# Kernel optimization log

Measured on AMD Instinct MI355X. Metric: run time of the kernel, lower is better.

Reference implementation:

```python
import jax, jax.numpy as jnp
import numpy as np

B, T, I, H, O = 64, 512, 256, 512, 10


def _init(key, shape, fan):
    k = 1.0 / np.sqrt(fan)
    return jax.random.uniform(key, shape, jnp.float32, -k, k)


def setup_inputs() -> dict:
    key = jax.random.key(0)
    ks = jax.random.split(key, 16)
    return {
        "x": jax.random.normal(ks[0], (B, T, I), jnp.float32),
        # LSTM params (PyTorch gate order: i, f, g, o)
        "lstm_w_ih": _init(ks[1], (4 * H, I), H),
        "lstm_w_hh": _init(ks[2], (4 * H, H), H),
        "lstm_b_ih": _init(ks[3], (4 * H,), H),
        "lstm_b_hh": _init(ks[4], (4 * H,), H),
        # GRU params (gate order: r, z, n)
        "gru_w_ih": _init(ks[5], (3 * H, H), H),
        "gru_w_hh": _init(ks[6], (3 * H, H), H),
        "gru_b_ih": _init(ks[7], (3 * H,), H),
        "gru_b_hh": _init(ks[8], (3 * H,), H),
        # RNN-tanh params
        "rnn_w_ih": _init(ks[9], (H, H), H),
        "rnn_w_hh": _init(ks[10], (H, H), H),
        "rnn_b_ih": _init(ks[11], (H,), H),
        "rnn_b_hh": _init(ks[12], (H,), H),
        # FC head
        "fc_w": _init(ks[13], (O, H), H),
        "fc_b": _init(ks[14], (O,), H),
    }


def _lstm(x, w_ih, w_hh, b_ih, b_hh):
    # Precompute input projections for all timesteps: [T, B, 4H]
    xg = (jnp.einsum('bti,gi->btg', x, w_ih) + b_ih + b_hh).transpose(1, 0, 2)
    h0 = jnp.zeros((x.shape[0], w_hh.shape[1]), x.dtype)

    def step(carry, xt):
        h, c = carry
        g = xt + h @ w_hh.T
        i, f, gg, o = jnp.split(g, 4, axis=-1)
        c = jax.nn.sigmoid(f) * c + jax.nn.sigmoid(i) * jnp.tanh(gg)
        h = jax.nn.sigmoid(o) * jnp.tanh(c)
        return (h, c), h

    _, hs = jax.lax.scan(step, (h0, h0), xg)
    return hs.transpose(1, 0, 2)  # [B, T, H]


def _gru(x, w_ih, w_hh, b_ih, b_hh):
    xg = (jnp.einsum('bti,gi->btg', x, w_ih) + b_ih).transpose(1, 0, 2)  # [T,B,3H]
    h0 = jnp.zeros((x.shape[0], w_hh.shape[1]), x.dtype)

    def step(h, xt):
        hg = h @ w_hh.T + b_hh
        xr, xz, xn = jnp.split(xt, 3, axis=-1)
        hr, hz, hn = jnp.split(hg, 3, axis=-1)
        r = jax.nn.sigmoid(xr + hr)
        z = jax.nn.sigmoid(xz + hz)
        n = jnp.tanh(xn + r * hn)
        h = (1.0 - z) * n + z * h
        return h, h

    _, hs = jax.lax.scan(step, h0, xg)
    return hs.transpose(1, 0, 2)


def _rnn_tanh(x, w_ih, w_hh, b_ih, b_hh):
    xg = (jnp.einsum('bti,gi->btg', x, w_ih) + b_ih + b_hh).transpose(1, 0, 2)
    h0 = jnp.zeros((x.shape[0], w_hh.shape[1]), x.dtype)

    def step(h, xt):
        h = jnp.tanh(xt + h @ w_hh.T)
        return h, h

    _, hs = jax.lax.scan(step, h0, xg)
    return hs.transpose(1, 0, 2)


def reference(x, lstm_w_ih, lstm_w_hh, lstm_b_ih, lstm_b_hh,
              gru_w_ih, gru_w_hh, gru_b_ih, gru_b_hh,
              rnn_w_ih, rnn_w_hh, rnn_b_ih, rnn_b_hh,
              fc_w, fc_b):
    h = _lstm(x, lstm_w_ih, lstm_w_hh, lstm_b_ih, lstm_b_hh)
    h = _gru(h, gru_w_ih, gru_w_hh, gru_b_ih, gru_b_hh)
    h = _rnn_tanh(h, rnn_w_ih, rnn_w_hh, rnn_b_ih, rnn_b_hh)
    last = h[:, -1]  # [B, H]
    return last @ fc_w.T + fc_b  # [B, O]
```

## Files before the change

### kernel.cpp

```cpp
#include <hip/hip_runtime.h>
#include <cstdint>

typedef _Float16 f16;
typedef _Float16 f16x8 __attribute__((ext_vector_type(8)));
typedef float f32x4 __attribute__((ext_vector_type(4)));
typedef unsigned u32;

#define DI static __device__ __forceinline__

constexpr int T = 512, H = 512, Osz = 10;
constexpr int NWG = 256, NTH = 768;
constexpr int GW = 32;
constexpr int GB = 8;
constexpr int BH = 64 * H;
constexpr size_t XH_OFF = 512 * 1024;
constexpr int XH_GRP = 8 * T * 256;

struct __align__(256) GSync { u32 cnt[2]; u32 epoch; u32 pad[61]; };

DI float sigf(float x)   { return 1.f / (1.f + __expf(-x)); }
DI float tanhf_(float x) { return 1.f - 2.f / (__expf(2.f * x) + 1.f); }

DI f16x8 cvt8(const float* p) {
  f16x8 r;
#pragma unroll
  for (int j = 0; j < 8; ++j) r[j] = (f16)p[j];
  return r;
}

DI void pin8(f16x8& v) { asm volatile("" : "+v"(v)); }

DI void st16_sc1(void* p, f16 v) {
  asm volatile("global_store_short %0, %1, off sc1" :: "v"(p), "v"(v));
}
DI void st32_sc1(void* p, u32 v) {
  asm volatile("global_store_dword %0, %1, off sc1" :: "v"(p), "v"(v));
}
DI void st128_sc1(void* p, f16x8 v) {
  asm volatile("global_store_dwordx4 %0, %1, off sc1" :: "v"(p), "v"(v));
}
DI void vm_drain() { asm volatile("s_waitcnt vmcnt(0)" ::: "memory"); }

DI void ld2_sc1(const void* p0, const void* p1, f16x8& a, f16x8& b) {
  asm volatile(
    "global_load_dwordx4 %0, %2, off sc1\n\t"
    "global_load_dwordx4 %1, %3, off sc1\n\t"
    "s_waitcnt vmcnt(0)"
    : "=&v"(a), "=&v"(b)
    : "v"(p0), "v"(p1)
    : "memory");
}

DI void ldrow8(const f16* base, f16x8* A) {
  asm volatile(
    "global_load_dwordx4 %0, %8, off sc1\n\t"
    "global_load_dwordx4 %1, %8, off offset:16 sc1\n\t"
    "global_load_dwordx4 %2, %8, off offset:32 sc1\n\t"
    "global_load_dwordx4 %3, %8, off offset:48 sc1\n\t"
    "global_load_dwordx4 %4, %8, off offset:64 sc1\n\t"
    "global_load_dwordx4 %5, %8, off offset:80 sc1\n\t"
    "global_load_dwordx4 %6, %8, off offset:96 sc1\n\t"
    "global_load_dwordx4 %7, %8, off offset:112 sc1\n\t"
    "s_waitcnt vmcnt(0)"
    : "=&v"(A[0]), "=&v"(A[1]), "=&v"(A[2]), "=&v"(A[3]),
      "=&v"(A[4]), "=&v"(A[5]), "=&v"(A[6]), "=&v"(A[7])
    : "v"(base)
    : "memory");
}

DI void group_barrier(GSync* g, u32 idx, int tid) {
  __syncthreads();
  if (tid == 0) {
    u32 old = __hip_atomic_fetch_add(&g->cnt[idx & 1], 1u,
                                     __ATOMIC_RELAXED, __HIP_MEMORY_SCOPE_AGENT);
    if (old == GW - 1) {
      __hip_atomic_store(&g->cnt[idx & 1], 0u, __ATOMIC_RELAXED, __HIP_MEMORY_SCOPE_AGENT);
      __hip_atomic_store(&g->epoch, idx + 1, __ATOMIC_RELAXED, __HIP_MEMORY_SCOPE_AGENT);
    } else {
      u32 spins = 0;
      while (__hip_atomic_load(&g->epoch, __ATOMIC_RELAXED, __HIP_MEMORY_SCOPE_AGENT) < idx + 1u) {
        __builtin_amdgcn_s_sleep(1);
        if (++spins > 1000000u) break;
      }
    }
  }
  __syncthreads();
}

__global__ __launch_bounds__(NTH, 1) void rnn_all(
    const float* __restrict__ x,
    const float* __restrict__ lwih, const float* __restrict__ lwhh,
    const float* __restrict__ lbih, const float* __restrict__ lbhh,
    const float* __restrict__ gwih, const float* __restrict__ gwhh,
    const float* __restrict__ gbih, const float* __restrict__ gbhh,
    const float* __restrict__ rwih, const float* __restrict__ rwhh,
    const float* __restrict__ rbih, const float* __restrict__ rbhh,
    const float* __restrict__ fcw, const float* __restrict__ fcb,
    float* __restrict__ out, char* __restrict__ ws)
{
  __shared__ __align__(16) u32 HSu[3 * 2048];
  __shared__ float P[12][16][20];
  __shared__ float sb[16][11];

  const int tid  = threadIdx.x;
  const int bid  = blockIdx.x;
  const int grp  = bid & 7;
  const int w32  = bid >> 3;
  const int bg0  = grp * GB;
  const int col0 = w32 * 16;
  const int w    = tid >> 6;
  const int lane = tid & 63;
  const int ln   = lane & 15;
  const int lk   = lane >> 4;

  GSync* gs = reinterpret_cast<GSync*>(ws) + grp;
  f16* HB = reinterpret_cast<f16*>(ws + 4096);
  f16* xh = reinterpret_cast<f16*>(ws + XH_OFF) + (size_t)grp * XH_GRP;

  f16x8 Bw[24];
#pragma unroll
  for (int ks = 16; ks < 24; ++ks) Bw[ks] = (f16x8)(f16)0.f;
  if (w < 4) {
    const int row = w * 512 + col0 + ln;
    const float* ph  = lwhh + (size_t)row * 512 + lk * 8;
    const float* px2 = lwih + (size_t)row * 256 + lk * 8;
#pragma unroll
    for (int ks = 0; ks < 16; ++ks) Bw[ks] = cvt8(ph + ks * 32);
#pragma unroll
    for (int ks = 0; ks < 8;  ++ks) Bw[16 + ks] = cvt8(px2 + ks * 32);
  } else if (w < 7) {
    const int row = (w - 4) * 512 + col0 + ln;
    const float* p = gwih + (size_t)row * 512 + lk * 8;
#pragma unroll
    for (int ks = 0; ks < 16; ++ks) Bw[ks] = cvt8(p + ks * 32);
  } else if (w < 10) {
    const int row = (w - 7) * 512 + col0 + ln;
    const float* p = gwhh + (size_t)row * 512 + lk * 8;
#pragma unroll
    for (int ks = 0; ks < 16; ++ks) Bw[ks] = cvt8(p + ks * 32);
  } else if (w == 10) {
    const float* p = rwhh + (size_t)(col0 + ln) * 512 + lk * 8;
#pragma unroll
    for (int ks = 0; ks < 16; ++ks) Bw[ks] = cvt8(p + ks * 32);
  } else {
    const float* p = rwih + (size_t)(col0 + ln) * 512 + lk * 8;
#pragma unroll
    for (int ks = 0; ks < 16; ++ks) Bw[ks] = cvt8(p + ks * 32);
  }
#pragma unroll
  for (int ks = 0; ks < 24; ++ks) pin8(Bw[ks]);

  for (int i = tid; i < 16 * 11; i += NTH) {
    int c = i / 11, j = i % 11, col = col0 + c;
    float v;
    if (j < 4)       v = lbih[j * 512 + col] + lbhh[j * 512 + col];
    else if (j < 7)  v = gbih[(j - 4) * 512 + col];
    else if (j < 10) v = gbhh[(j - 7) * 512 + col];
    else             v = rbih[col] + rbhh[col];
    sb[c][j] = v;
  }

  {
    const float* xg_ = x + (size_t)bg0 * (T * 256);
    for (int c = w32 * NTH + tid; c < XH_GRP / 8; c += GW * NTH) {
      const float* p = xg_ + (size_t)c * 8;
      f16x8 v;
#pragma unroll
      for (int j = 0; j < 8; ++j) v[j] = (f16)p[j];
      st128_sc1((void*)(xh + (size_t)c * 8), v);
    }
  }
  {
    int i = w32 * NTH + tid;
    if (i < 12288) {
      int buf = i >> 12, r = i & 4095, par = r >> 11, row = (r >> 8) & 7, cu = r & 255;
      void* p = (void*)(HB + (size_t)buf * 2 * BH + (size_t)par * BH
                           + (size_t)(bg0 + row) * H + cu * 2);
      st32_sc1(p, 0u);
    }
  }
  vm_drain();

  group_barrier(gs, 0u, tid);

  float creg = 0.f, hgreg = 0.f;

  const int hbuf = (w < 7) ? 0 : ((w == 10) ? 2 : 1);
  const f16* xrow = xh + ((size_t)(ln & 7) << 17) + lk * 8;

#pragma unroll 1
  for (int s = 0; s <= T + 1; ++s) {
    const int cur = s & 1, prev = cur ^ 1;
    const int sc = (s < T) ? s : (T - 1);

    {
      int s0 = tid, s1 = tid + NTH;
      int b0 = s0 >> 9, r0 = s0 & 511, row0 = r0 >> 6, sr0 = r0 & 63;
      int b1 = s1 >> 9, r1 = s1 & 511, row1 = r1 >> 6, sr1 = r1 & 63;
      const f16* p0 = HB + (size_t)b0 * 2 * BH + (size_t)prev * BH
                         + (size_t)(bg0 + row0) * H + sr0 * 8;
      const f16* p1 = HB + (size_t)b1 * 2 * BH + (size_t)prev * BH
                         + (size_t)(bg0 + row1) * H + sr1 * 8;
      f16x8 va, vb;
      ld2_sc1(p0, p1, va, vb);
      *reinterpret_cast<f16x8*>(&HSu[(b0 << 11) + row0 * 256 + ((sr0 ^ row0) << 2)]) = va;
      *reinterpret_cast<f16x8*>(&HSu[(b1 << 11) + row1 * 256 + ((sr1 ^ row1) << 2)]) = vb;
    }
    __syncthreads();

    const u32 rw_ = (u32)(ln & 7);
    const u32 abase = (u32)hbuf * 2048u + rw_ * 256u;

    f32x4 acc = {0.f, 0.f, 0.f, 0.f};
    if (w < 4) {
      const f16* px = xrow + (size_t)sc * 256;
#pragma unroll
      for (int ks = 0; ks < 8; ++ks) {
        const f16x8 a = *reinterpret_cast<const f16x8*>(px + ks * 32);
        acc = __builtin_amdgcn_mfma_f32_16x16x32_f16(a, Bw[16 + ks], acc, 0, 0, 0);
      }
    }
#pragma unroll
    for (int ks = 0; ks < 16; ++ks) {
      const f16x8 a = *reinterpret_cast<const f16x8*>(
          &HSu[abase + ((((u32)(ks * 4 + lk)) ^ rw_) << 2)]);
      acc = __builtin_amdgcn_mfma_f32_16x16x32_f16(a, Bw[ks], acc, 0, 0, 0);
    }

    if (lk < 2)
      *reinterpret_cast<f32x4*>(&P[w][ln][lk * 4]) = acc;
    __syncthreads();

    if (tid < 128) {
      const int cb = tid >> 4, cc = tid & 15;
      const int gb = bg0 + cb, col = col0 + cc;

      float iL = sigf(P[0][cc][cb] + sb[cc][0]);
      float fL = sigf(P[1][cc][cb] + sb[cc][1]);
      float gL = tanhf_(P[2][cc][cb] + sb[cc][2]);
      float oL = sigf(P[3][cc][cb] + sb[cc][3]);
      float cn = fL * creg + iL * gL;
      float hLv = oL * tanhf_(cn);
      float xr = P[4][cc][cb] + sb[cc][4];
      float xz = P[5][cc][cb] + sb[cc][5];
      float xn = P[6][cc][cb] + sb[cc][6];
      float hr = P[7][cc][cb] + sb[cc][7];
      float hz = P[8][cc][cb] + sb[cc][8];
      float hn = P[9][cc][cb] + sb[cc][9];
      float rg = sigf(xr + hr), zg = sigf(xz + hz);
      float ng = tanhf_(xn + rg * hn);
      float hGv = (1.f - zg) * ng + zg * hgreg;
      float hRv = tanhf_(P[10][cc][cb] + P[11][cc][cb] + sb[cc][10]);

      f16* rowp = HB + (size_t)cur * BH + (size_t)gb * H + col;
      if (s < T)            { creg = cn; st16_sc1((void*)rowp, (f16)hLv); }
      if (s >= 1 && s <= T) { hgreg = hGv; st16_sc1((void*)(rowp + 2 * BH), (f16)hGv); }
      if (s >= 2)           st16_sc1((void*)(rowp + 4 * BH), (f16)hRv);
      vm_drain();
    }
    group_barrier(gs, (u32)(s + 1), tid);
  }

  if (w32 == 0 && tid < 640) {
    const f16* hlast = HB + 4 * BH + BH;
    int bo = tid >> 3, kq = tid & 7;
    int bl = bo / 10, o = bo % 10;
    const f16* ph = hlast + (size_t)(bg0 + bl) * H + kq * 64;
    const float* pw = fcw + (size_t)o * H + kq * 64;
    f16x8 v[8];
    ldrow8(ph, v);
    float a = 0.f;
#pragma unroll
    for (int q = 0; q < 8; ++q)
#pragma unroll
      for (int j = 0; j < 8; ++j) a += (float)v[q][j] * pw[q * 8 + j];
    a += __shfl_xor(a, 1);
    a += __shfl_xor(a, 2);
    a += __shfl_xor(a, 4);
    if (kq == 0) out[(bg0 + bl) * Osz + o] = a + fcb[o];
  }
}

extern "C" void kernel_launch(void* const* d_in, const int* in_sizes, int n_in,
                              void* d_out, int out_size, void* d_ws, size_t ws_size,
                              hipStream_t stream) {
  (void)in_sizes; (void)n_in; (void)out_size; (void)ws_size;
  const float* x    = (const float*)d_in[0];
  const float* lwih = (const float*)d_in[1];
  const float* lwhh = (const float*)d_in[2];
  const float* lbih = (const float*)d_in[3];
  const float* lbhh = (const float*)d_in[4];
  const float* gwih = (const float*)d_in[5];
  const float* gwhh = (const float*)d_in[6];
  const float* gbih = (const float*)d_in[7];
  const float* gbhh = (const float*)d_in[8];
  const float* rwih = (const float*)d_in[9];
  const float* rwhh = (const float*)d_in[10];
  const float* rbih = (const float*)d_in[11];
  const float* rbhh = (const float*)d_in[12];
  const float* fcw  = (const float*)d_in[13];
  const float* fcb  = (const float*)d_in[14];
  float* outp = (float*)d_out;
  char* wsp   = (char*)d_ws;

  hipMemsetAsync(d_ws, 0, 4096, stream);

  rnn_all<<<dim3(NWG), dim3(NTH), 0, stream>>>(
      x, lwih, lwhh, lbih, lbhh, gwih, gwhh, gbih, gbhh,
      rwih, rwhh, rbih, rbhh, fcw, fcb, outp, wsp);
}
```

Measured before the change: 2.009 ms.

## Replace atomic counter group barrier with per-block slot flags and stage x in LDS

```diff
diff --git a/kernel.cpp b/kernel.cpp
--- a/kernel.cpp
+++ b/kernel.cpp
@@ -5,6 +5,7 @@
 typedef _Float16 f16x8 __attribute__((ext_vector_type(8)));
 typedef float f32x4 __attribute__((ext_vector_type(4)));
 typedef unsigned u32;
+typedef u32 u32x4 __attribute__((ext_vector_type(4)));
 
 #define DI static __device__ __forceinline__
 
@@ -16,8 +17,6 @@
 constexpr size_t XH_OFF = 512 * 1024;
 constexpr int XH_GRP = 8 * T * 256;
 
-struct __align__(256) GSync { u32 cnt[2]; u32 epoch; u32 pad[61]; };
-
 DI float sigf(float x)   { return 1.f / (1.f + __expf(-x)); }
 DI float tanhf_(float x) { return 1.f - 2.f / (__expf(2.f * x) + 1.f); }
 
@@ -29,6 +28,7 @@
 }
 
 DI void pin8(f16x8& v) { asm volatile("" : "+v"(v)); }
+DI u32 umin_(u32 a, u32 b) { return a < b ? a : b; }
 
 DI void st16_sc1(void* p, f16 v) {
   asm volatile("global_store_short %0, %1, off sc1" :: "v"(p), "v"(v));
@@ -48,6 +48,17 @@
     "s_waitcnt vmcnt(0)"
     : "=&v"(a), "=&v"(b)
     : "v"(p0), "v"(p1)
+    : "memory");
+}
+DI void ld3_sc1(const void* p0, const void* p1, const void* p2,
+                f16x8& a, f16x8& b, f16x8& c) {
+  asm volatile(
+    "global_load_dwordx4 %0, %3, off sc1\n\t"
+    "global_load_dwordx4 %1, %4, off sc1\n\t"
+    "global_load_dwordx4 %2, %5, off sc1\n\t"
+    "s_waitcnt vmcnt(0)"
+    : "=&v"(a), "=&v"(b), "=&v"(c)
+    : "v"(p0), "v"(p1), "v"(p2)
     : "memory");
 }
 
@@ -68,20 +79,39 @@
     : "memory");
 }
 
-DI void group_barrier(GSync* g, u32 idx, int tid) {
+DI u32 slots_min(const u32* base) {
+  u32x4 a0, a1, a2, a3, a4, a5, a6, a7;
+  asm volatile(
+    "global_load_dwordx4 %0, %8, off sc1\n\t"
+    "global_load_dwordx4 %1, %8, off offset:16 sc1\n\t"
+    "global_load_dwordx4 %2, %8, off offset:32 sc1\n\t"
+    "global_load_dwordx4 %3, %8, off offset:48 sc1\n\t"
+    "global_load_dwordx4 %4, %8, off offset:64 sc1\n\t"
+    "global_load_dwordx4 %5, %8, off offset:80 sc1\n\t"
+    "global_load_dwordx4 %6, %8, off offset:96 sc1\n\t"
+    "global_load_dwordx4 %7, %8, off offset:112 sc1\n\t"
+    "s_waitcnt vmcnt(0)"
+    : "=&v"(a0), "=&v"(a1), "=&v"(a2), "=&v"(a3),
+      "=&v"(a4), "=&v"(a5), "=&v"(a6), "=&v"(a7)
+    : "v"(base)
+    : "memory");
+  u32 m = 0xFFFFFFFFu;
+#define MIN4_(v) m = umin_(m, umin_(umin_(v[0], v[1]), umin_(v[2], v[3])))
+  MIN4_(a0); MIN4_(a1); MIN4_(a2); MIN4_(a3);
+  MIN4_(a4); MIN4_(a5); MIN4_(a6); MIN4_(a7);
+#undef MIN4_
+  return m;
+}
+
+DI void barrier_arrive(u32* slots, int w32, u32 val, int tid) {
   __syncthreads();
+  if (tid == 0) st32_sc1(&slots[w32], val);
+}
+DI void barrier_wait(u32* slots, u32 target, int tid) {
   if (tid == 0) {
-    u32 old = __hip_atomic_fetch_add(&g->cnt[idx & 1], 1u,
-                                     __ATOMIC_RELAXED, __HIP_MEMORY_SCOPE_AGENT);
-    if (old == GW - 1) {
-      __hip_atomic_store(&g->cnt[idx & 1], 0u, __ATOMIC_RELAXED, __HIP_MEMORY_SCOPE_AGENT);
-      __hip_atomic_store(&g->epoch, idx + 1, __ATOMIC_RELAXED, __HIP_MEMORY_SCOPE_AGENT);
-    } else {
-      u32 spins = 0;
-      while (__hip_atomic_load(&g->epoch, __ATOMIC_RELAXED, __HIP_MEMORY_SCOPE_AGENT) < idx + 1u) {
-        __builtin_amdgcn_s_sleep(1);
-        if (++spins > 1000000u) break;
-      }
+    u32 spins = 0;
+    while (slots_min(slots) < target) {
+      if (++spins > 300000u) break;
     }
   }
   __syncthreads();
@@ -99,6 +129,7 @@
     float* __restrict__ out, char* __restrict__ ws)
 {
   __shared__ __align__(16) u32 HSu[3 * 2048];
+  __shared__ __align__(16) u32 XS[1024];
   __shared__ float P[12][16][20];
   __shared__ float sb[16][11];
 
@@ -113,7 +144,7 @@
   const int ln   = lane & 15;
   const int lk   = lane >> 4;
 
-  GSync* gs = reinterpret_cast<GSync*>(ws) + grp;
+  u32* slots = reinterpret_cast<u32*>(ws) + (size_t)grp * 64;
   f16* HB = reinterpret_cast<f16*>(ws + 4096);
   f16* xh = reinterpret_cast<f16*>(ws + XH_OFF) + (size_t)grp * XH_GRP;
 
@@ -181,15 +212,16 @@
   }
   vm_drain();
 
-  group_barrier(gs, 0u, tid);
+  barrier_arrive(slots, w32, 1u, tid);
 
   float creg = 0.f, hgreg = 0.f;
 
   const int hbuf = (w < 7) ? 0 : ((w == 10) ? 2 : 1);
-  const f16* xrow = xh + ((size_t)(ln & 7) << 17) + lk * 8;
 
 #pragma unroll 1
   for (int s = 0; s <= T + 1; ++s) {
+    barrier_wait(slots, (u32)(s + 1), tid);
+
     const int cur = s & 1, prev = cur ^ 1;
     const int sc = (s < T) ? s : (T - 1);
 
@@ -202,7 +234,16 @@
       const f16* p1 = HB + (size_t)b1 * 2 * BH + (size_t)prev * BH
                          + (size_t)(bg0 + row1) * H + sr1 * 8;
       f16x8 va, vb;
-      ld2_sc1(p0, p1, va, vb);
+      if (w < 4) {
+        int xrow = tid >> 5, xsr = tid & 31;
+        const f16* p2 = xh + ((size_t)xrow << 17) + (size_t)sc * 256 + xsr * 8;
+        f16x8 vc;
+        ld3_sc1(p0, p1, p2, va, vb, vc);
+        *reinterpret_cast<f16x8*>(
+            &XS[(((u32)xrow << 5) | ((u32)(xsr ^ xrow))) << 2]) = vc;
+      } else {
+        ld2_sc1(p0, p1, va, vb);
+      }
       *reinterpret_cast<f16x8*>(&HSu[(b0 << 11) + row0 * 256 + ((sr0 ^ row0) << 2)]) = va;
       *reinterpret_cast<f16x8*>(&HSu[(b1 << 11) + row1 * 256 + ((sr1 ^ row1) << 2)]) = vb;
     }
@@ -213,10 +254,10 @@
 
     f32x4 acc = {0.f, 0.f, 0.f, 0.f};
     if (w < 4) {
-      const f16* px = xrow + (size_t)sc * 256;
 #pragma unroll
       for (int ks = 0; ks < 8; ++ks) {
-        const f16x8 a = *reinterpret_cast<const f16x8*>(px + ks * 32);
+        const f16x8 a = *reinterpret_cast<const f16x8*>(
+            &XS[(((rw_ << 5) | (((u32)(ks * 4 + lk)) ^ rw_)) << 2)]);
         acc = __builtin_amdgcn_mfma_f32_16x16x32_f16(a, Bw[16 + ks], acc, 0, 0, 0);
       }
     }
@@ -258,26 +299,29 @@
       if (s >= 2)           st16_sc1((void*)(rowp + 4 * BH), (f16)hRv);
       vm_drain();
     }
-    group_barrier(gs, (u32)(s + 1), tid);
-  }
-
-  if (w32 == 0 && tid < 640) {
-    const f16* hlast = HB + 4 * BH + BH;
-    int bo = tid >> 3, kq = tid & 7;
-    int bl = bo / 10, o = bo % 10;
-    const f16* ph = hlast + (size_t)(bg0 + bl) * H + kq * 64;
-    const float* pw = fcw + (size_t)o * H + kq * 64;
-    f16x8 v[8];
-    ldrow8(ph, v);
-    float a = 0.f;
-#pragma unroll
-    for (int q = 0; q < 8; ++q)
-#pragma unroll
-      for (int j = 0; j < 8; ++j) a += (float)v[q][j] * pw[q * 8 + j];
-    a += __shfl_xor(a, 1);
-    a += __shfl_xor(a, 2);
-    a += __shfl_xor(a, 4);
-    if (kq == 0) out[(bg0 + bl) * Osz + o] = a + fcb[o];
+    barrier_arrive(slots, w32, (u32)(s + 2), tid);
+  }
+
+  if (w32 == 0) {
+    barrier_wait(slots, (u32)(T + 3), tid);
+    if (tid < 640) {
+      const f16* hlast = HB + 4 * BH + BH;
+      int bo = tid >> 3, kq = tid & 7;
+      int bl = bo / 10, o = bo % 10;
+      const f16* ph = hlast + (size_t)(bg0 + bl) * H + kq * 64;
+      const float* pw = fcw + (size_t)o * H + kq * 64;
+      f16x8 v[8];
+      ldrow8(ph, v);
+      float a = 0.f;
+#pragma unroll
+      for (int q = 0; q < 8; ++q)
+#pragma unroll
+        for (int j = 0; j < 8; ++j) a += (float)v[q][j] * pw[q * 8 + j];
+      a += __shfl_xor(a, 1);
+      a += __shfl_xor(a, 2);
+      a += __shfl_xor(a, 4);
+      if (kq == 0) out[(bg0 + bl) * Osz + o] = a + fcb[o];
+    }
   }
 }
 
```

After: 2.075 ms. 1.03x slower.

## Split each workgroup's batch into two interleaved groups to hide barrier latency

Applied to the files above, without the earlier changes.

```diff
diff --git a/kernel.cpp b/kernel.cpp
--- a/kernel.cpp
+++ b/kernel.cpp
@@ -11,10 +11,9 @@
 constexpr int T = 512, H = 512, Osz = 10;
 constexpr int NWG = 256, NTH = 768;
 constexpr int GW = 32;
-constexpr int GB = 8;
+constexpr int GB = 4;
 constexpr int BH = 64 * H;
 constexpr size_t XH_OFF = 512 * 1024;
-constexpr int XH_GRP = 8 * T * 256;
 
 struct __align__(256) GSync { u32 cnt[2]; u32 epoch; u32 pad[61]; };
 
@@ -41,14 +40,11 @@
 }
 DI void vm_drain() { asm volatile("s_waitcnt vmcnt(0)" ::: "memory"); }
 
-DI void ld2_sc1(const void* p0, const void* p1, f16x8& a, f16x8& b) {
-  asm volatile(
-    "global_load_dwordx4 %0, %2, off sc1\n\t"
-    "global_load_dwordx4 %1, %3, off sc1\n\t"
-    "s_waitcnt vmcnt(0)"
-    : "=&v"(a), "=&v"(b)
-    : "v"(p0), "v"(p1)
-    : "memory");
+DI f16x8 ld1_sc1(const void* p) {
+  f16x8 a;
+  asm volatile("global_load_dwordx4 %0, %1, off sc1\n\ts_waitcnt vmcnt(0)"
+               : "=v"(a) : "v"(p) : "memory");
+  return a;
 }
 
 DI void ldrow8(const f16* base, f16x8* A) {
@@ -68,7 +64,7 @@
     : "memory");
 }
 
-DI void group_barrier(GSync* g, u32 idx, int tid) {
+DI void g_arrive(GSync* g, u32 idx, int tid) {
   __syncthreads();
   if (tid == 0) {
     u32 old = __hip_atomic_fetch_add(&g->cnt[idx & 1], 1u,
@@ -76,12 +72,15 @@
     if (old == GW - 1) {
       __hip_atomic_store(&g->cnt[idx & 1], 0u, __ATOMIC_RELAXED, __HIP_MEMORY_SCOPE_AGENT);
       __hip_atomic_store(&g->epoch, idx + 1, __ATOMIC_RELAXED, __HIP_MEMORY_SCOPE_AGENT);
-    } else {
-      u32 spins = 0;
-      while (__hip_atomic_load(&g->epoch, __ATOMIC_RELAXED, __HIP_MEMORY_SCOPE_AGENT) < idx + 1u) {
-        __builtin_amdgcn_s_sleep(1);
-        if (++spins > 1000000u) break;
-      }
+    }
+  }
+}
+DI void g_wait(GSync* g, u32 idx, int tid) {
+  if (tid == 0) {
+    u32 spins = 0;
+    while (__hip_atomic_load(&g->epoch, __ATOMIC_RELAXED, __HIP_MEMORY_SCOPE_AGENT) < idx + 1u) {
+      __builtin_amdgcn_s_sleep(1);
+      if (++spins > 1000000u) break;
     }
   }
   __syncthreads();
@@ -98,24 +97,28 @@
     const float* __restrict__ fcw, const float* __restrict__ fcb,
     float* __restrict__ out, char* __restrict__ ws)
 {
-  __shared__ __align__(16) u32 HSu[3 * 2048];
+  __shared__ __align__(16) u32 HSA[3 * 1024];
+  __shared__ __align__(16) u32 HSB[3 * 1024];
   __shared__ float P[12][16][20];
   __shared__ float sb[16][11];
 
   const int tid  = threadIdx.x;
   const int bid  = blockIdx.x;
-  const int grp  = bid & 7;
+  const int grpA = bid & 7;
+  const int grpB = grpA + 8;
   const int w32  = bid >> 3;
-  const int bg0  = grp * GB;
+  const int bg0A = grpA * GB;
+  const int bg0B = grpB * GB;
   const int col0 = w32 * 16;
   const int w    = tid >> 6;
   const int lane = tid & 63;
   const int ln   = lane & 15;
   const int lk   = lane >> 4;
 
-  GSync* gs = reinterpret_cast<GSync*>(ws) + grp;
+  GSync* gsA = reinterpret_cast<GSync*>(ws) + grpA;
+  GSync* gsB = reinterpret_cast<GSync*>(ws) + grpB;
   f16* HB = reinterpret_cast<f16*>(ws + 4096);
-  f16* xh = reinterpret_cast<f16*>(ws + XH_OFF) + (size_t)grp * XH_GRP;
+  f16* xh = reinterpret_cast<f16*>(ws + XH_OFF);
 
   f16x8 Bw[24];
 #pragma unroll
@@ -161,64 +164,52 @@
   }
 
   {
-    const float* xg_ = x + (size_t)bg0 * (T * 256);
-    for (int c = w32 * NTH + tid; c < XH_GRP / 8; c += GW * NTH) {
-      const float* p = xg_ + (size_t)c * 8;
-      f16x8 v;
-#pragma unroll
-      for (int j = 0; j < 8; ++j) v[j] = (f16)p[j];
+    const int g0 = bid * NTH + tid;
+    for (int c = g0; c < 64 * T * 256 / 8; c += NWG * NTH) {
+      f16x8 v = cvt8(x + (size_t)c * 8);
       st128_sc1((void*)(xh + (size_t)c * 8), v);
     }
-  }
-  {
-    int i = w32 * NTH + tid;
-    if (i < 12288) {
-      int buf = i >> 12, r = i & 4095, par = r >> 11, row = (r >> 8) & 7, cu = r & 255;
-      void* p = (void*)(HB + (size_t)buf * 2 * BH + (size_t)par * BH
-                           + (size_t)(bg0 + row) * H + cu * 2);
-      st32_sc1(p, 0u);
-    }
+    if (g0 < 3 * 2 * BH / 2)
+      st32_sc1((void*)(reinterpret_cast<u32*>(HB) + g0), 0u);
   }
   vm_drain();
-
-  group_barrier(gs, 0u, tid);
-
-  float creg = 0.f, hgreg = 0.f;
+  g_arrive(gsA, 0u, tid);
+  g_arrive(gsB, 0u, tid);
+
+  float cregA = 0.f, hgregA = 0.f, cregB = 0.f, hgregB = 0.f;
 
   const int hbuf = (w < 7) ? 0 : ((w == 10) ? 2 : 1);
-  const f16* xrow = xh + ((size_t)(ln & 7) << 17) + lk * 8;
-
-#pragma unroll 1
-  for (int s = 0; s <= T + 1; ++s) {
+
+  const int sb0 = tid >> 8;
+  const int sr_ = tid & 255;
+  const int srow = sr_ >> 6;
+  const int sslt = sr_ & 63;
+  const size_t stg_off = (size_t)sb0 * 2 * BH + (size_t)srow * H + sslt * 8;
+  const u32 lds_off = (u32)((sb0 << 10) + srow * 256 + ((sslt ^ srow) << 2));
+
+  const u32 rw_ = (u32)(ln & 3);
+  const u32 abase = (u32)hbuf * 1024u + rw_ * 256u;
+
+  auto do_phase = [&](u32* HSu, GSync* gs, const int bg0,
+                      float& creg, float& hgreg, const int s) {
     const int cur = s & 1, prev = cur ^ 1;
     const int sc = (s < T) ? s : (T - 1);
 
+    g_wait(gs, (u32)s, tid);
+
     {
-      int s0 = tid, s1 = tid + NTH;
-      int b0 = s0 >> 9, r0 = s0 & 511, row0 = r0 >> 6, sr0 = r0 & 63;
-      int b1 = s1 >> 9, r1 = s1 & 511, row1 = r1 >> 6, sr1 = r1 & 63;
-      const f16* p0 = HB + (size_t)b0 * 2 * BH + (size_t)prev * BH
-                         + (size_t)(bg0 + row0) * H + sr0 * 8;
-      const f16* p1 = HB + (size_t)b1 * 2 * BH + (size_t)prev * BH
-                         + (size_t)(bg0 + row1) * H + sr1 * 8;
-      f16x8 va, vb;
-      ld2_sc1(p0, p1, va, vb);
-      *reinterpret_cast<f16x8*>(&HSu[(b0 << 11) + row0 * 256 + ((sr0 ^ row0) << 2)]) = va;
-      *reinterpret_cast<f16x8*>(&HSu[(b1 << 11) + row1 * 256 + ((sr1 ^ row1) << 2)]) = vb;
+      const f16* p0 = HB + stg_off + (size_t)prev * BH + (size_t)bg0 * H;
+      *reinterpret_cast<f16x8*>(&HSu[lds_off]) = ld1_sc1(p0);
     }
     __syncthreads();
 
-    const u32 rw_ = (u32)(ln & 7);
-    const u32 abase = (u32)hbuf * 2048u + rw_ * 256u;
-
     f32x4 acc = {0.f, 0.f, 0.f, 0.f};
+    f16x8 xa[8];
     if (w < 4) {
-      const f16* px = xrow + (size_t)sc * 256;
-#pragma unroll
-      for (int ks = 0; ks < 8; ++ks) {
-        const f16x8 a = *reinterpret_cast<const f16x8*>(px + ks * 32);
-        acc = __builtin_amdgcn_mfma_f32_16x16x32_f16(a, Bw[16 + ks], acc, 0, 0, 0);
-      }
+      const f16* px = xh + ((size_t)(bg0 + (ln & 3)) * T + sc) * 256 + lk * 8;
+#pragma unroll
+      for (int ks = 0; ks < 8; ++ks)
+        xa[ks] = *reinterpret_cast<const f16x8*>(px + ks * 32);
     }
 #pragma unroll
     for (int ks = 0; ks < 16; ++ks) {
@@ -226,12 +217,16 @@
           &HSu[abase + ((((u32)(ks * 4 + lk)) ^ rw_) << 2)]);
       acc = __builtin_amdgcn_mfma_f32_16x16x32_f16(a, Bw[ks], acc, 0, 0, 0);
     }
-
-    if (lk < 2)
-      *reinterpret_cast<f32x4*>(&P[w][ln][lk * 4]) = acc;
+    if (w < 4) {
+#pragma unroll
+      for (int ks = 0; ks < 8; ++ks)
+        acc = __builtin_amdgcn_mfma_f32_16x16x32_f16(xa[ks], Bw[16 + ks], acc, 0, 0, 0);
+    }
+    if (lk == 0)
+      *reinterpret_cast<f32x4*>(&P[w][ln][0]) = acc;
     __syncthreads();
 
-    if (tid < 128) {
+    if (tid < 64) {
       const int cb = tid >> 4, cc = tid & 15;
       const int gb = bg0 + cb, col = col0 + cc;
 
@@ -258,14 +253,23 @@
       if (s >= 2)           st16_sc1((void*)(rowp + 4 * BH), (f16)hRv);
       vm_drain();
     }
-    group_barrier(gs, (u32)(s + 1), tid);
-  }
-
+    g_arrive(gs, (u32)(s + 1), tid);
+  };
+
+#pragma unroll 1
+  for (int s = 0; s <= T + 1; ++s) {
+    do_phase(HSA, gsA, bg0A, cregA, hgregA, s);
+    do_phase(HSB, gsB, bg0B, cregB, hgregB, s);
+  }
+
+  g_wait(gsA, (u32)(T + 2), tid);
+  g_wait(gsB, (u32)(T + 2), tid);
   if (w32 == 0 && tid < 640) {
     const f16* hlast = HB + 4 * BH + BH;
     int bo = tid >> 3, kq = tid & 7;
     int bl = bo / 10, o = bo % 10;
-    const f16* ph = hlast + (size_t)(bg0 + bl) * H + kq * 64;
+    int row = (bl < 4) ? (bg0A + bl) : (bg0B + bl - 4);
+    const f16* ph = hlast + (size_t)row * H + kq * 64;
     const float* pw = fcw + (size_t)o * H + kq * 64;
     f16x8 v[8];
     ldrow8(ph, v);
@@ -277,7 +281,7 @@
     a += __shfl_xor(a, 1);
     a += __shfl_xor(a, 2);
     a += __shfl_xor(a, 4);
-    if (kq == 0) out[(bg0 + bl) * Osz + o] = a + fcb[o];
+    if (kq == 0) out[row * Osz + o] = a + fcb[o];
   }
 }
 
```

New measurement: 5.512 ms. 2.74x slower.
